# Kernel tuning notes

Hardware: AMD Instinct MI355X
Metric: run time of the kernel (lower is better)

The kernel has to match this reference:

```python
import jax, jax.numpy as jnp
import numpy as np

DIM = 2048
HEAD_DIM = 64
N_HEADS = 16
N_KV_HEADS = 4
RANK = 8
ALPHA = 16
LORA_SCALE = ALPHA / RANK  # 2.0
SEQ = 2048
BATCH = 1
ROPE_THETA = 10000.0


def setup_inputs() -> dict:
    key = jax.random.key(0)
    ks = jax.random.split(key, 12)
    std = 0.02
    x = jax.random.normal(ks[0], (BATCH, SEQ, DIM), dtype=jnp.float32)
    # rope tables: (SEQ, HEAD_DIM//2, 2) = (cos, sin)
    inv_freq = 1.0 / (ROPE_THETA ** (jnp.arange(0, HEAD_DIM, 2, dtype=jnp.float32) / HEAD_DIM))
    ang = jnp.arange(SEQ, dtype=jnp.float32)[:, None] * inv_freq[None, :]
    freq_cis = jnp.stack([jnp.cos(ang), jnp.sin(ang)], axis=-1)
    mk = lambda k, shp: (jax.random.normal(k, shp, dtype=jnp.float32) * std)
    return {
        "x": x,
        "freq_cis": freq_cis,
        "wq": mk(ks[1], (HEAD_DIM, DIM)),
        "wq_a": mk(ks[2], (RANK, DIM)),
        "wq_b": mk(ks[3], (N_HEADS * HEAD_DIM, RANK)),
        "wk": mk(ks[4], (HEAD_DIM, DIM)),
        "wk_a": mk(ks[5], (RANK, DIM)),
        "wk_b": mk(ks[6], (N_KV_HEADS * HEAD_DIM, RANK)),
        "wv": mk(ks[7], (HEAD_DIM, DIM)),
        "wv_a": mk(ks[8], (RANK, DIM)),
        "wv_b": mk(ks[9], (N_KV_HEADS * HEAD_DIM, RANK)),
        "wo": mk(ks[10], (DIM, HEAD_DIM)),
        "wo_share": mk(ks[11], (DIM, N_HEADS * HEAD_DIM)),
    }


def _shared_plus_lora(x, w_base, w_a, w_b, n_heads):
    # base: single head (B,S,HEAD_DIM) broadcast across heads; LoRA adds per-head delta
    base = jnp.einsum('bsd,hd->bsh', x, w_base)                    # (B,S,Dh)
    delta = jnp.einsum('bsr,or->bso', jnp.einsum('bsd,rd->bsr', x, w_a), w_b) * LORA_SCALE
    B, S, _ = x.shape
    delta = delta.reshape(B, S, n_heads, HEAD_DIM)
    return base[:, :, None, :] + delta                             # (B,S,H,Dh)


def _rope(t, freq_cis):
    # t: (B,S,H,Dh); freq_cis: (S, Dh//2, 2)
    B, S, H, D = t.shape
    tr = t.reshape(B, S, H, D // 2, 2)
    cos = freq_cis[:, None, :, 0]  # (S,1,Dh//2)
    sin = freq_cis[:, None, :, 1]
    xr, xi = tr[..., 0], tr[..., 1]
    out = jnp.stack([xr * cos - xi * sin, xr * sin + xi * cos], axis=-1)
    return out.reshape(B, S, H, D)


def reference(x, freq_cis, wq, wq_a, wq_b, wk, wk_a, wk_b, wv, wv_a, wv_b, wo, wo_share):
    B, S, _ = x.shape
    g = N_HEADS // N_KV_HEADS
    xq = _shared_plus_lora(x, wq, wq_a, wq_b, N_HEADS)      # (B,S,H,Dh)
    xk = _shared_plus_lora(x, wk, wk_a, wk_b, N_KV_HEADS)   # (B,S,Hkv,Dh)
    xv = _shared_plus_lora(x, wv, wv_a, wv_b, N_KV_HEADS)
    xq = _rope(xq, freq_cis[:S])
    xk = _rope(xk, freq_cis[:S])
    # GQA attention without materializing repeat_kv: group q heads per kv head
    q = xq.reshape(B, S, N_KV_HEADS, g, HEAD_DIM)
    scale = 1.0 / jnp.sqrt(jnp.asarray(HEAD_DIM, dtype=x.dtype))
    scores = jnp.einsum('bskgd,btkd->bkgst', q, xk) * scale  # (B,Hkv,g,S,S)
    causal = jnp.tril(jnp.ones((S, S), dtype=bool))
    scores = jnp.where(causal, scores, jnp.asarray(-jnp.inf, dtype=scores.dtype))
    p = jax.nn.softmax(scores, axis=-1)
    out = jnp.einsum('bkgst,btkd->bskgd', p, xv).reshape(B, S, N_HEADS, HEAD_DIM)
    # output projection: shared base applied per-head then summed + LoRA-style shared delta
    base = jnp.einsum('bshd,ed->bse', out, wo)
    delta = jnp.einsum('bsf,ef->bse', out.reshape(B, S, N_HEADS * HEAD_DIM), wo_share)
    return base + delta
```

## Files before the change

### kernel.cpp

```cpp
#include <hip/hip_runtime.h>
#include <hip/hip_bf16.h>

#define DEV __device__ __forceinline__

typedef unsigned short u16;
typedef __attribute__((ext_vector_type(8))) short short8;
typedef __attribute__((ext_vector_type(4))) float f32x4;
typedef __attribute__((ext_vector_type(16))) float f32x16;

DEV u16 f2bf(float f) {
  union { float f; unsigned u; } v; v.f = f;
  unsigned r = v.u + 0x7FFFu + ((v.u >> 16) & 1u);
  return (u16)(r >> 16);
}

DEV unsigned cvtpk(float lo, float hi) {
  unsigned r;
  asm("v_cvt_pk_bf16_f32 %0, %1, %2" : "=v"(r) : "v"(lo), "v"(hi));
  return r;
}

DEV void async_ld16(const u16* g, u16* l) {
  __builtin_amdgcn_global_load_lds((__attribute__((address_space(1))) void*)g,
                                   (__attribute__((address_space(3))) void*)l,
                                   16, 0, 0);
}

DEV f32x4 mfma16(short8 a, short8 b, f32x4 c) {
  return __builtin_amdgcn_mfma_f32_16x16x32_bf16(a, b, c, 0, 0, 0);
}
DEV f32x16 mfma32(short8 a, short8 b, f32x16 c) {
  return __builtin_amdgcn_mfma_f32_32x32x16_bf16(a, b, c, 0, 0, 0);
}

DEV short8 mkfrag(unsigned w0, unsigned w1, unsigned w2, unsigned w3) {
  union { unsigned u[4]; short8 s; } u;
  u.u[0] = w0; u.u[1] = w1; u.u[2] = w2; u.u[3] = w3;
  return u.s;
}

DEV short8 lds_rd(const u16* buf, int row, int colb) {
  return *(const short8*)((const char*)buf + row*128 + (colb ^ ((row & 7) << 4)));
}

#define QSCALE (0.125f * 1.4426950408889634f)

__global__ __launch_bounds__(256) void k_prep(const float* __restrict__ x,
    const float* __restrict__ wq, const float* __restrict__ wk,
    const float* __restrict__ wv, const float* __restrict__ wqa,
    const float* __restrict__ wka, const float* __restrict__ wva,
    const float* __restrict__ wo, const float* __restrict__ wos,
    u16* __restrict__ xb, u16* __restrict__ W1, u16* __restrict__ Weff) {
  const int bid = blockIdx.x;
  if (bid < 1024) {
    int i = bid*256 + threadIdx.x;
    for (; i < 1048576; i += 1024*256) {
      float4 v = ((const float4*)x)[i];
      ushort4 o;
      o.x = f2bf(v.x); o.y = f2bf(v.y); o.z = f2bf(v.z); o.w = f2bf(v.w);
      ((ushort4*)xb)[i] = o;
    }
  } else if (bid < 1280) {
    const int row = bid - 1024;
    const float* src = nullptr; float sc = 1.f;
    if (row < 64)       { src = wq  + row*2048;       sc = QSCALE; }
    else if (row < 128) { src = wk  + (row-64)*2048;  }
    else if (row < 192) { src = wv  + (row-128)*2048; }
    else if (row < 200) { src = wqa + (row-192)*2048; sc = 2.f*QSCALE; }
    else if (row < 208) { src = wka + (row-200)*2048; sc = 2.f; }
    else if (row < 216) { src = wva + (row-208)*2048; sc = 2.f; }
    for (int c = threadIdx.x; c < 2048; c += 256)
      W1[row*2048 + c] = src ? f2bf(src[c]*sc) : (u16)0;
  } else {
    const int e = bid - 1280;
    for (int f = threadIdx.x; f < 1024; f += 256)
      Weff[e*1024 + f] = f2bf(wos[e*1024 + f] + wo[e*64 + (f & 63)]);
  }
}

template<int BM, int BN>
__global__ __launch_bounds__(512)
void k_gemm_bt(const u16* __restrict__ A, const u16* __restrict__ B,
               float* __restrict__ C, int M, int N, int K, int kslice) {
  constexpr int NWC = (BN >= 128) ? 4 : 2;
  constexpr int NWR = 8 / NWC;
  constexpr int WM = BM / NWR, WN = BN / NWC;
  constexpr int FM = WM/16, FN = WN/16;
  __shared__ u16 As[BM*64];
  __shared__ u16 Bs[BN*64];
  const int tid = threadIdx.x;
  const int w = tid >> 6, l = tid & 63;
  const int wm = (w / NWC)*WM, wn = (w % NWC)*WN;
  const int tm = blockIdx.y*BM, tn = blockIdx.x*BN;
  const int k0 = blockIdx.z * kslice;
  C += (size_t)blockIdx.z * M * N;
  const int sr = (w << 3) + (l >> 3);
  const int sc = (((l & 7) ^ (l >> 3)) << 3);
  const int la = l & 15, lg = l >> 4;

  f32x4 acc[FM][FN];
#pragma unroll
  for (int i = 0; i < FM; ++i)
#pragma unroll
    for (int j = 0; j < FN; ++j) acc[i][j] = (f32x4){0.f,0.f,0.f,0.f};

  const int nk = kslice >> 6;
  for (int kt = 0; kt < nk; ++kt) {
    const int kk = k0 + (kt << 6);
#pragma unroll
    for (int j = 0; j < BM/64; ++j)
      async_ld16(A + (size_t)(tm + j*64 + sr)*K + kk + sc, &As[(j*64 + w*8)*64]);
#pragma unroll
    for (int j = 0; j < BN/64; ++j)
      async_ld16(B + (size_t)(tn + j*64 + sr)*K + kk + sc, &Bs[(j*64 + w*8)*64]);
    __syncthreads();
    short8 af[FM][2], bfr[FN][2];
#pragma unroll
    for (int mi = 0; mi < FM; ++mi)
#pragma unroll
      for (int ks = 0; ks < 2; ++ks)
        af[mi][ks] = lds_rd(As, wm + mi*16 + la, ks*64 + lg*16);
#pragma unroll
    for (int ni = 0; ni < FN; ++ni)
#pragma unroll
      for (int ks = 0; ks < 2; ++ks)
        bfr[ni][ks] = lds_rd(Bs, wn + ni*16 + la, ks*64 + lg*16);
#pragma unroll
    for (int ks = 0; ks < 2; ++ks)
#pragma unroll
      for (int mi = 0; mi < FM; ++mi)
#pragma unroll
        for (int ni = 0; ni < FN; ++ni)
          acc[mi][ni] = mfma16(af[mi][ks], bfr[ni][ks], acc[mi][ni]);
    __syncthreads();
  }
#pragma unroll
  for (int mi = 0; mi < FM; ++mi)
#pragma unroll
    for (int ni = 0; ni < FN; ++ni) {
      const int r0 = tm + wm + mi*16 + lg*4;
      const int cc = tn + wn + ni*16 + la;
#pragma unroll
      for (int r = 0; r < 4; ++r)
        C[(size_t)(r0 + r)*N + cc] = acc[mi][ni][r];
    }
}

__global__ __launch_bounds__(256)
void k_expand(const float* __restrict__ proj, const float* __restrict__ wqb,
              const float* __restrict__ wkb, const float* __restrict__ wvb,
              const float* __restrict__ freq, u16* __restrict__ Q,
              u16* __restrict__ Kb, u16* __restrict__ Vt) {
  __shared__ float prs[256];
  const int s = blockIdx.x;
  {
    const int c = threadIdx.x;
    const float* p0 = proj + s*256;
    float t0 = (p0[c]             + p0[c +  524288]) + (p0[c + 1048576] + p0[c + 1572864]);
    float t1 = (p0[c + 2097152] + p0[c + 2621440]) + (p0[c + 3145728] + p0[c + 3670016]);
    prs[c] = t0 + t1;
  }
  __syncthreads();
  const int d = threadIdx.x & 63;
  const int w = threadIdx.x >> 6;
  const float cs = freq[s*64 + (d & 62)];
  const float sn = freq[s*64 + (d & 62) + 1];
#pragma unroll
  for (int pass = 0; pass < 6; ++pass) {
    const int slot = pass*4 + w;
    int bcol, tb; const float* wb;
    if (slot < 16)      { bcol = 0;   tb = 192; wb = wqb + (slot*64 + d)*8; }
    else if (slot < 20) { bcol = 64;  tb = 200; wb = wkb + ((slot-16)*64 + d)*8; }
    else                { bcol = 128; tb = 208; wb = wvb + ((slot-20)*64 + d)*8; }
    float val = prs[bcol + d];
#pragma unroll
    for (int r = 0; r < 8; ++r) val += prs[tb + r] * wb[r];
    if (slot < 20) {
      float partner = __shfl_xor(val, 1);
      val = (d & 1) ? (partner*sn + val*cs) : (val*cs - partner*sn);
    }
    u16 o = f2bf(val);
    if (slot < 16)      Q [((size_t)slot*2048 + s)*64 + d] = o;
    else if (slot < 20) Kb[((size_t)(slot-16)*2048 + s)*64 + d] = o;
    else                Vt[(size_t)(slot-20)*131072 + (size_t)d*2048 + s] = o;
  }
}

__global__ __launch_bounds__(256, 4)
void k_attn(const u16* __restrict__ Q, const u16* __restrict__ Kb,
            const u16* __restrict__ Vt, u16* __restrict__ O) {
  __shared__ __align__(16) char smem[33792];
  const int w = threadIdx.x >> 6, l = threadIdx.x & 63;
  const int bid = blockIdx.x;
  const int h = bid & 15, kh = h >> 2;
  const int z = bid >> 4;
  const int a = z & 15, b = z >> 4;
  const int qs = (b << 4) | ((b & 1) ? (15 - a) : a);
  const int q0 = qs*32;
  const int lq = l & 31, hh = l >> 5;
  const int qg = q0 + lq;

  u16* kbuf = (u16*)(smem + w*8192);
  u16* vbuf = (u16*)(smem + w*8192 + 4096);

  const u16* Qh = Q  + (size_t)h *131072;
  const u16* Kh = Kb + (size_t)kh*131072;
  const u16* Vh = Vt + (size_t)kh*131072;

  short8 bq[4];
#pragma unroll
  for (int ks = 0; ks < 4; ++ks)
    bq[ks] = *(const short8*)&Qh[qg*64 + ks*16 + hh*8];

  f32x16 acc0, acc1;
#pragma unroll
  for (int r = 0; r < 16; ++r) { acc0[r] = 0.f; acc1[r] = 0.f; }
  float lsum = 0.f;
  const float SM = 20.f;

  const int nt = qs + 1;

#define STAGE_K(T0)                                                       \
  {                                                                       \
    const int t0_ = (T0);                                                 \
    _Pragma("unroll")                                                     \
    for (int j = 0; j < 4; ++j) {                                         \
      const int c = j*64 + l;                                             \
      const int row = c >> 3, e = (c & 7) ^ (row & 7);                    \
      async_ld16(Kh + (size_t)(t0_ + row)*64 + e*8, kbuf + j*512);        \
    }                                                                     \
  }
#define STAGE_V(T0)                                                       \
  {                                                                       \
    const int t0_ = (T0);                                                 \
    _Pragma("unroll")                                                     \
    for (int j = 0; j < 4; ++j) {                                         \
      const int c = j*64 + l;                                             \
      const int row = c >> 3, e = (c & 7) ^ (row & 7);                    \
      const int dd = row + (e >> 2)*32;                                   \
      async_ld16(Vh + (size_t)dd*2048 + t0_ + (e & 3)*8, vbuf + j*512);   \
    }                                                                     \
  }

  if (w < nt) { STAGE_K(w*32); STAGE_V(w*32); }

  for (int tt = w; tt < nt; tt += 4) {
    asm volatile("s_waitcnt vmcnt(0)" ::: "memory");
    __builtin_amdgcn_sched_barrier(0);
    short8 ak[4];
#pragma unroll
    for (int ks = 0; ks < 4; ++ks)
      ak[ks] = lds_rd(kbuf, lq, ks*32 + hh*16);
    asm volatile("s_waitcnt lgkmcnt(0)" ::: "memory");
    __builtin_amdgcn_sched_barrier(0);
    if (tt + 4 < nt) STAGE_K((tt + 4)*32);

    f32x16 s;
#pragma unroll
    for (int r = 0; r < 16; ++r) s[r] = 0.f;
    __builtin_amdgcn_s_setprio(1);
#pragma unroll
    for (int ks = 0; ks < 4; ++ks)
      s = mfma32(ak[ks], bq[ks], s);
    __builtin_amdgcn_s_setprio(0);

    const int t0 = tt*32;
    if (t0 + 31 > q0) {
#pragma unroll
      for (int r = 0; r < 16; ++r) {
        const int tl = (r & 3) + ((r >> 2) << 3) + (hh << 2);
        if (t0 + tl > qg) s[r] = -1e30f;
      }
    }

    short8 av[2][2];
#pragma unroll
    for (int dh = 0; dh < 2; ++dh)
#pragma unroll
      for (int k2 = 0; k2 < 2; ++k2)
        av[dh][k2] = lds_rd(vbuf, lq, (dh*4 + k2*2 + hh)*16);

    unsigned cw[4][2];
    float psum = 0.f;
#pragma unroll
    for (int rq = 0; rq < 4; ++rq) {
      float a0 = exp2f(s[4*rq+0] - SM), a1 = exp2f(s[4*rq+1] - SM);
      float a2 = exp2f(s[4*rq+2] - SM), a3 = exp2f(s[4*rq+3] - SM);
      psum += (a0 + a1) + (a2 + a3);
      cw[rq][0] = cvtpk(a0, a1); cw[rq][1] = cvtpk(a2, a3);
    }
    lsum += psum;

    asm volatile("s_waitcnt lgkmcnt(0)" ::: "memory");
    __builtin_amdgcn_sched_barrier(0);
    if (tt + 4 < nt) STAGE_V((tt + 4)*32);

    unsigned y00 = __shfl_xor(hh ? cw[0][0] : cw[1][0], 32);
    unsigned y01 = __shfl_xor(hh ? cw[0][1] : cw[1][1], 32);
    unsigned y10 = __shfl_xor(hh ? cw[2][0] : cw[3][0], 32);
    unsigned y11 = __shfl_xor(hh ? cw[2][1] : cw[3][1], 32);
    short8 p0 = hh ? mkfrag(y00, y01, cw[1][0], cw[1][1])
                   : mkfrag(cw[0][0], cw[0][1], y00, y01);
    short8 p1 = hh ? mkfrag(y10, y11, cw[3][0], cw[3][1])
                   : mkfrag(cw[2][0], cw[2][1], y10, y11);

    __builtin_amdgcn_s_setprio(1);
    acc0 = mfma32(av[0][0], p0, acc0);
    acc1 = mfma32(av[1][0], p0, acc1);
    acc0 = mfma32(av[0][1], p1, acc0);
    acc1 = mfma32(av[1][1], p1, acc1);
    __builtin_amdgcn_s_setprio(0);
  }
#undef STAGE_K
#undef STAGE_V

  __syncthreads();
  float* comb = (float*)smem;
  u16* scr = (u16*)(smem + 26624);
  if (w > 0) {
    float* cb = comb + ((w-1)*64 + l)*33;
#pragma unroll
    for (int r = 0; r < 16; ++r) { cb[r] = acc0[r]; cb[16+r] = acc1[r]; }
    cb[32] = lsum;
  }
  __syncthreads();
  if (w == 0) {
#pragma unroll
    for (int j = 0; j < 3; ++j) {
      const float* cb = comb + (j*64 + l)*33;
#pragma unroll
      for (int r = 0; r < 16; ++r) { acc0[r] += cb[r]; acc1[r] += cb[16+r]; }
      lsum += cb[32];
    }
    lsum += __shfl_xor(lsum, 32);
    const float inv = 1.f / lsum;
#pragma unroll
    for (int dt = 0; dt < 2; ++dt)
#pragma unroll
      for (int rq = 0; rq < 4; ++rq) {
        float v0 = (dt ? acc1[4*rq+0] : acc0[4*rq+0]) * inv;
        float v1 = (dt ? acc1[4*rq+1] : acc0[4*rq+1]) * inv;
        float v2 = (dt ? acc1[4*rq+2] : acc0[4*rq+2]) * inv;
        float v3 = (dt ? acc1[4*rq+3] : acc0[4*rq+3]) * inv;
        const int dby = dt*64 + rq*16 + hh*8;
        const int by = lq*128 + (dby ^ ((lq & 7) << 4));
        *(unsigned*)((char*)scr + by)     = cvtpk(v0, v1);
        *(unsigned*)((char*)scr + by + 4) = cvtpk(v2, v3);
      }
#pragma unroll
    for (int qq = 0; qq < 4; ++qq) {
      const int qrow = qq*8 + (l >> 3);
      const int by = qrow*128 + (((l & 7) << 4) ^ ((qrow & 7) << 4));
      short8 v = *(const short8*)((const char*)scr + by);
      *(short8*)&O[(size_t)(q0 + qrow)*1024 + h*64 + (l & 7)*8] = v;
    }
  }
}

extern "C" void kernel_launch(void* const* d_in, const int* in_sizes, int n_in,
                              void* d_out, int out_size, void* d_ws, size_t ws_size,
                              hipStream_t stream) {
  const float* x    = (const float*)d_in[0];
  const float* freq = (const float*)d_in[1];
  const float* wq   = (const float*)d_in[2];
  const float* wqa  = (const float*)d_in[3];
  const float* wqb  = (const float*)d_in[4];
  const float* wk   = (const float*)d_in[5];
  const float* wka  = (const float*)d_in[6];
  const float* wkb  = (const float*)d_in[7];
  const float* wv   = (const float*)d_in[8];
  const float* wva  = (const float*)d_in[9];
  const float* wvb  = (const float*)d_in[10];
  const float* wo   = (const float*)d_in[11];
  const float* wos  = (const float*)d_in[12];
  float* out = (float*)d_out;

  char* ws = (char*)d_ws;
  u16*  x_bf = (u16*)ws;
  u16*  Qb   = (u16*)ws;
  u16*  Kbuf = (u16*)(ws + (4u<<20));
  u16*  Vtb  = (u16*)(ws + (5u<<20));
  u16*  W1   = (u16*)(ws + (8u<<20));
  u16*  Weff = (u16*)(ws + (9u<<20));
  float* proj = (float*)(ws + (13u<<20));
  u16*  Obf  = (u16*)(ws + (13u<<20));

  k_prep    <<<3328, 256, 0, stream>>>(x, wq, wk, wv, wqa, wka, wva, wo, wos,
                                       x_bf, W1, Weff);
  k_gemm_bt<128,64><<<dim3(4,16,8), 512, 0, stream>>>(x_bf, W1, proj, 2048, 256, 2048, 256);
  k_expand  <<<dim3(2048), 256, 0, stream>>>(proj, wqb, wkb, wvb, freq, Qb, Kbuf, Vtb);
  k_attn    <<<dim3(1024), 256, 0, stream>>>(Qb, Kbuf, Vtb, Obf);
  k_gemm_bt<64,128><<<dim3(16,32,1), 512, 0, stream>>>(Obf, Weff, out, 2048, 2048, 1024, 1024);
}
```

Baseline: 79.86 us.

## Shrink GEMM blocks to 256 threads and split attention K/V wait counts

The GEMM kernel moves from 512 to 256 threads per block with min-waves launch bounds. The first projection GEMM now uses 64x64 tiles across more blocks. LDS fragments are loaded per k-step to cut register pressure, and the staging swizzle is recomputed per row. In attention, the single full vmcnt(0) wait becomes separate partial waits for K and V, so the K tile can be consumed while the V prefetch is still in flight. This trades larger per-wave work and a more delicate wait-count ordering for higher occupancy and more overlap.

```diff
diff --git a/kernel.cpp b/kernel.cpp
--- a/kernel.cpp
+++ b/kernel.cpp
@@ -78,12 +78,12 @@
   }
 }
 
-template<int BM, int BN>
-__global__ __launch_bounds__(512)
+template<int BM, int BN, int MINW>
+__global__ __launch_bounds__(256, MINW)
 void k_gemm_bt(const u16* __restrict__ A, const u16* __restrict__ B,
                float* __restrict__ C, int M, int N, int K, int kslice) {
   constexpr int NWC = (BN >= 128) ? 4 : 2;
-  constexpr int NWR = 8 / NWC;
+  constexpr int NWR = 4 / NWC;
   constexpr int WM = BM / NWR, WN = BN / NWC;
   constexpr int FM = WM/16, FN = WN/16;
   __shared__ u16 As[BM*64];
@@ -94,8 +94,7 @@
   const int tm = blockIdx.y*BM, tn = blockIdx.x*BN;
   const int k0 = blockIdx.z * kslice;
   C += (size_t)blockIdx.z * M * N;
-  const int sr = (w << 3) + (l >> 3);
-  const int sc = (((l & 7) ^ (l >> 3)) << 3);
+  const int srw = (w << 3) + (l >> 3);
   const int la = l & 15, lg = l >> 4;
 
   f32x4 acc[FM][FN];
@@ -108,30 +107,33 @@
   for (int kt = 0; kt < nk; ++kt) {
     const int kk = k0 + (kt << 6);
 #pragma unroll
-    for (int j = 0; j < BM/64; ++j)
-      async_ld16(A + (size_t)(tm + j*64 + sr)*K + kk + sc, &As[(j*64 + w*8)*64]);
-#pragma unroll
-    for (int j = 0; j < BN/64; ++j)
-      async_ld16(B + (size_t)(tn + j*64 + sr)*K + kk + sc, &Bs[(j*64 + w*8)*64]);
+    for (int j = 0; j < BM/32; ++j) {
+      const int row = j*32 + srw;
+      const int e = (((l & 7) ^ (row & 7)) << 3);
+      async_ld16(A + (size_t)(tm + row)*K + kk + e, &As[(j*32 + (w << 3))*64]);
+    }
+#pragma unroll
+    for (int j = 0; j < BN/32; ++j) {
+      const int row = j*32 + srw;
+      const int e = (((l & 7) ^ (row & 7)) << 3);
+      async_ld16(B + (size_t)(tn + row)*K + kk + e, &Bs[(j*32 + (w << 3))*64]);
+    }
     __syncthreads();
-    short8 af[FM][2], bfr[FN][2];
-#pragma unroll
-    for (int mi = 0; mi < FM; ++mi)
-#pragma unroll
-      for (int ks = 0; ks < 2; ++ks)
-        af[mi][ks] = lds_rd(As, wm + mi*16 + la, ks*64 + lg*16);
-#pragma unroll
-    for (int ni = 0; ni < FN; ++ni)
-#pragma unroll
-      for (int ks = 0; ks < 2; ++ks)
-        bfr[ni][ks] = lds_rd(Bs, wn + ni*16 + la, ks*64 + lg*16);
-#pragma unroll
-    for (int ks = 0; ks < 2; ++ks)
+#pragma unroll
+    for (int ks = 0; ks < 2; ++ks) {
+      short8 af[FM], bfr[FN];
 #pragma unroll
       for (int mi = 0; mi < FM; ++mi)
+        af[mi] = lds_rd(As, wm + mi*16 + la, ks*64 + lg*16);
+#pragma unroll
+      for (int ni = 0; ni < FN; ++ni)
+        bfr[ni] = lds_rd(Bs, wn + ni*16 + la, ks*64 + lg*16);
+#pragma unroll
+      for (int mi = 0; mi < FM; ++mi)
 #pragma unroll
         for (int ni = 0; ni < FN; ++ni)
-          acc[mi][ni] = mfma16(af[mi][ks], bfr[ni][ks], acc[mi][ni]);
+          acc[mi][ni] = mfma16(af[mi], bfr[ni], acc[mi][ni]);
+    }
     __syncthreads();
   }
 #pragma unroll
@@ -245,7 +247,7 @@
   if (w < nt) { STAGE_K(w*32); STAGE_V(w*32); }
 
   for (int tt = w; tt < nt; tt += 4) {
-    asm volatile("s_waitcnt vmcnt(0)" ::: "memory");
+    asm volatile("s_waitcnt vmcnt(4)" ::: "memory");
     __builtin_amdgcn_sched_barrier(0);
     short8 ak[4];
 #pragma unroll
@@ -253,7 +255,8 @@
       ak[ks] = lds_rd(kbuf, lq, ks*32 + hh*16);
     asm volatile("s_waitcnt lgkmcnt(0)" ::: "memory");
     __builtin_amdgcn_sched_barrier(0);
-    if (tt + 4 < nt) STAGE_K((tt + 4)*32);
+    const bool restage = (tt + 4 < nt);
+    if (restage) STAGE_K((tt + 4)*32);
 
     f32x16 s;
 #pragma unroll
@@ -273,6 +276,9 @@
       }
     }
 
+    if (restage) { asm volatile("s_waitcnt vmcnt(4)" ::: "memory"); }
+    else         { asm volatile("s_waitcnt vmcnt(0)" ::: "memory"); }
+    __builtin_amdgcn_sched_barrier(0);
     short8 av[2][2];
 #pragma unroll
     for (int dh = 0; dh < 2; ++dh)
@@ -293,7 +299,7 @@
 
     asm volatile("s_waitcnt lgkmcnt(0)" ::: "memory");
     __builtin_amdgcn_sched_barrier(0);
-    if (tt + 4 < nt) STAGE_V((tt + 4)*32);
+    if (restage) STAGE_V((tt + 4)*32);
 
     unsigned y00 = __shfl_xor(hh ? cw[0][0] : cw[1][0], 32);
     unsigned y01 = __shfl_xor(hh ? cw[0][1] : cw[1][1], 32);
@@ -387,8 +393,8 @@
 
   k_prep    <<<3328, 256, 0, stream>>>(x, wq, wk, wv, wqa, wka, wva, wo, wos,
                                        x_bf, W1, Weff);
-  k_gemm_bt<128,64><<<dim3(4,16,8), 512, 0, stream>>>(x_bf, W1, proj, 2048, 256, 2048, 256);
+  k_gemm_bt<64,64,6><<<dim3(4,32,8), 256, 0, stream>>>(x_bf, W1, proj, 2048, 256, 2048, 256);
   k_expand  <<<dim3(2048), 256, 0, stream>>>(proj, wqb, wkb, wvb, freq, Qb, Kbuf, Vtb);
   k_attn    <<<dim3(1024), 256, 0, stream>>>(Qb, Kbuf, Vtb, Obf);
-  k_gemm_bt<64,128><<<dim3(16,32,1), 512, 0, stream>>>(Obf, Weff, out, 2048, 2048, 1024, 1024);
-}
+  k_gemm_bt<64,128,5><<<dim3(16,32,1), 256, 0, stream>>>(Obf, Weff, out, 2048, 2048, 1024, 1024);
+}
```

Measured after the change: 81.79 us. 1.02x slower.
